# Performance work log

Measured on AMD Instinct MI355X. Metric: run time of the kernel, lower is better.

## Reference

```python
import jax, jax.numpy as jnp
import numpy as np

D_MODEL = 1024
N_HEADS = 16
HEAD_DIM = D_MODEL // N_HEADS
WINDOW = 256


def setup_inputs() -> dict:
    key = jax.random.key(0)
    k1, k2, k3 = jax.random.split(key, 3)
    B, T = 4, 2048
    x = jax.random.normal(k1, (B, T, D_MODEL), dtype=jnp.float32)
    # weights stored as [in, out] (torch Linear does x @ W.T with W [out,in])
    scale_qkv = 1.0 / np.sqrt(D_MODEL)
    w_qkv = jax.random.normal(k2, (D_MODEL, 3 * D_MODEL), dtype=jnp.float32) * scale_qkv
    w_out = jax.random.normal(k3, (D_MODEL, D_MODEL), dtype=jnp.float32) * scale_qkv
    return {"x": x, "w_qkv": w_qkv, "w_out": w_out}


def _sliding_window_attention(x, w_qkv, w_out):
    B, T, C = x.shape
    qkv = x @ w_qkv                              # [B,T,3C]
    q, k, v = jnp.split(qkv, 3, axis=-1)

    def reshape(t):
        return t.reshape(B, T, N_HEADS, HEAD_DIM).transpose(0, 2, 1, 3)  # [B,H,T,Dh]

    q, k, v = reshape(q), reshape(k), reshape(v)

    # banded causal mask: position i attends to j in [i-WINDOW, i]
    pos = jnp.arange(T)
    dist = pos[None, :] - pos[:, None]           # dist[i,j] = j - i
    blocked = (dist > 0) | (dist < -WINDOW)      # True = blocked

    scale = 1.0 / np.sqrt(HEAD_DIM)
    scores = jnp.einsum('bhqd,bhkd->bhqk', q, k) * scale
    scores = jnp.where(blocked[None, None], -jnp.inf, scores)
    attn = jax.nn.softmax(scores, axis=-1)
    out = jnp.einsum('bhqk,bhkd->bhqd', attn, v)
    out = out.transpose(0, 2, 1, 3).reshape(B, T, C)
    return out @ w_out


def reference(x, w_qkv, w_out):
    return _sliding_window_attention(x, w_qkv, w_out)
```

## Files before the change

### kernel.cpp

```cpp
#include <hip/hip_runtime.h>
#include <stdint.h>

#define D_MODEL 1024
#define NHEADS  16
#define WINDOW  256
#define BATCH   4
#define SEQ     2048
#define NROWS   (BATCH*SEQ)

using short8 = __attribute__((ext_vector_type(8))) short;
using f32x4  = __attribute__((ext_vector_type(4))) float;
using u32x4  = __attribute__((ext_vector_type(4))) uint32_t;
using u16x4  = __attribute__((ext_vector_type(4))) unsigned short;
typedef unsigned short u16;

__device__ __forceinline__ u16 f2b(float f) {
  union { float f; uint32_t u; } v; v.f = f;
  uint32_t r = v.u + 0x7fffu + ((v.u >> 16) & 1u);
  return (u16)(r >> 16);
}

__device__ __forceinline__ void gload_lds16(const void* g, void* l) {
  __builtin_amdgcn_global_load_lds(
      (const __attribute__((address_space(1))) uint32_t*)g,
      (__attribute__((address_space(3))) uint32_t*)l, 16, 0, 0);
}

__global__ void cvt_cast_kernel(const float* __restrict__ in, u16* __restrict__ out, int n4) {
  int i = blockIdx.x * blockDim.x + threadIdx.x;
  if (i < n4) {
    f32x4 v = *(const f32x4*)(in + 4 * (size_t)i);
    u16x4 o;
    o.x = f2b(v.x); o.y = f2b(v.y); o.z = f2b(v.z); o.w = f2b(v.w);
    *(u16x4*)(out + 4 * (size_t)i) = o;
  }
}

__global__ __launch_bounds__(256) void cvtT_kernel(const float* __restrict__ in, u16* __restrict__ out,
                                                   int K, int C) {
  __shared__ float T[64 * 65];
  const int nbn = C >> 6;
  const int bn = blockIdx.x % nbn, bk = blockIdx.x / nbn;
  const int tid = threadIdx.x;
#pragma unroll
  for (int it = 0; it < 4; ++it) {
    int c = it * 256 + tid;
    int k = c >> 4, g = c & 15;
    f32x4 v = *(const f32x4*)&in[(size_t)(bk * 64 + k) * C + bn * 64 + g * 4];
#pragma unroll
    for (int j = 0; j < 4; ++j) T[k * 65 + g * 4 + j] = v[j];
  }
  __syncthreads();
#pragma unroll
  for (int it = 0; it < 4; ++it) {
    int c = it * 256 + tid;
    int n = c >> 4, kg = c & 15;
    u16x4 o;
#pragma unroll
    for (int j = 0; j < 4; ++j) o[j] = f2b(T[(kg * 4 + j) * 65 + n]);
    *(u16x4*)&out[(size_t)(bn * 64 + n) * K + bk * 64 + kg * 4] = o;
  }
}

template <int MODE>
__global__ __launch_bounds__(256) void gemm97_kernel(
    const u16* __restrict__ A, const u16* __restrict__ BT,
    u16* __restrict__ qk, u16* __restrict__ vT, float* __restrict__ outf,
    int M, int N, int K, int nbx) {
  __shared__ short SM[3 * 8192];

  const int tid = threadIdx.x;
  const int l = tid & 63;
  const int w = tid >> 6;
  const int lr = l & 15, g = l >> 4;
  const int wr = w >> 1, wc = w & 1;

  const int nwg = gridDim.x;
  const int lid = blockIdx.x;
  const int wg = (lid & 7) * (nwg >> 3) + (lid >> 3);
  const int bx = wg % nbx, by = wg / nbx;
  const int m0 = by * 128, n0 = bx * 128;

  const int ko = (g ^ (lr & 3)) * 8;
  const int NKT = K >> 5;

  const int c0 = tid, c1 = 256 + tid;
  const int r0 = c0 >> 2, g0 = (c0 & 3) ^ (r0 & 3);
  const int r1 = c1 >> 2, g1 = (c1 & 3) ^ (r1 & 3);

  f32x4 acc[4][4] = {};

  auto stage = [&](int slot, int kt) {
    const int kk = kt << 5;
    short* As = SM + slot * 8192;
    short* Bs = As + 4096;
    gload_lds16(A  + (size_t)(m0 + r0) * K + kk + g0 * 8, &As[(w * 64) * 8]);
    gload_lds16(A  + (size_t)(m0 + r1) * K + kk + g1 * 8, &As[(256 + w * 64) * 8]);
    gload_lds16(BT + (size_t)(n0 + r0) * K + kk + g0 * 8, &Bs[(w * 64) * 8]);
    gload_lds16(BT + (size_t)(n0 + r1) * K + kk + g1 * 8, &Bs[(256 + w * 64) * 8]);
  };

  stage(0, 0);
  stage(1, 1);

  int slot = 0;
  for (int t = 0; t < NKT; ++t) {
    if (t == NKT - 1) { asm volatile("s_waitcnt vmcnt(0)" ::: "memory"); }
    else              { asm volatile("s_waitcnt vmcnt(4)" ::: "memory"); }
    __builtin_amdgcn_s_barrier();
    if (t + 2 < NKT) {
      int s2 = slot + 2; if (s2 >= 3) s2 -= 3;
      stage(s2, t + 2);
    }
    const short* As = SM + slot * 8192;
    const short* Bs = As + 4096;
    short8 af[4], bf[4];
#pragma unroll
    for (int fm = 0; fm < 4; ++fm)
      af[fm] = *(const short8*)&As[(wr * 64 + fm * 16 + lr) * 32 + ko];
#pragma unroll
    for (int fn = 0; fn < 4; ++fn)
      bf[fn] = *(const short8*)&Bs[(wc * 64 + fn * 16 + lr) * 32 + ko];
#pragma unroll
    for (int fm = 0; fm < 4; ++fm)
#pragma unroll
      for (int fn = 0; fn < 4; ++fn)
        acc[fm][fn] = __builtin_amdgcn_mfma_f32_16x16x32_bf16(af[fm], bf[fn], acc[fm][fn], 0, 0, 0);
    slot = (slot + 1 == 3) ? 0 : slot + 1;
  }

  if (MODE == 1) {
#pragma unroll
    for (int fm = 0; fm < 4; ++fm) {
      const int m = m0 + wr * 64 + fm * 16 + (l >> 4) * 4;
#pragma unroll
      for (int fn = 0; fn < 4; ++fn) {
        const int n = n0 + wc * 64 + fn * 16 + lr;
#pragma unroll
        for (int r = 0; r < 4; ++r)
          outf[(size_t)(m + r) * N + n] = acc[fm][fn][r];
      }
    }
    return;
  }

  if (n0 < 2048) {
#pragma unroll
    for (int fm = 0; fm < 4; ++fm) {
      const int m = m0 + wr * 64 + fm * 16 + (l >> 4) * 4;
#pragma unroll
      for (int fn = 0; fn < 4; ++fn) {
        const int n = n0 + wc * 64 + fn * 16 + lr;
#pragma unroll
        for (int r = 0; r < 4; ++r)
          qk[(size_t)(m + r) * 2048 + n] = f2b(acc[fm][fn][r]);
      }
    }
  } else {
    __syncthreads();
    short* Tw = SM + w * 1152;
    const int b = by >> 4;
    const int h = (n0 - 2048 + wc * 64) >> 6;
    const int t0 = (by & 15) * 128 + wr * 64;
    const size_t dbase = ((size_t)(b * NHEADS + h)) * 64;
#pragma unroll
    for (int fn = 0; fn < 4; ++fn) {
#pragma unroll
      for (int fm = 0; fm < 4; ++fm)
#pragma unroll
        for (int r = 0; r < 4; ++r)
          Tw[lr * 72 + fm * 16 + (l >> 4) * 4 + r] = (short)f2b(acc[fm][fn][r]);
      asm volatile("s_waitcnt lgkmcnt(0)" ::: "memory");
#pragma unroll
      for (int it = 0; it < 2; ++it) {
        int c = it * 64 + l;
        int row = c >> 3, off = (c & 7) * 8;
        short8 v = *(const short8*)&Tw[row * 72 + off];
        *(short8*)&vT[(dbase + fn * 16 + row) * 2048 + t0 + off] = v;
      }
      asm volatile("s_waitcnt lgkmcnt(0)" ::: "memory");
    }
  }
}

__global__ __launch_bounds__(256) void attn_kernel(
    const u16* __restrict__ qk, const u16* __restrict__ vT, u16* __restrict__ attn) {
  __shared__ short Ks[2][64 * 72];
  __shared__ short Vs[2][64 * 72];
  __shared__ short Ps[4 * 16 * 72];

  const int tid = threadIdx.x;
  const int l = tid & 63;
  const int w = tid >> 6;

  const int lid = blockIdx.x;
  const int xcd = lid & 7, slot = lid >> 3;
  const int bh = (slot >> 5) * 8 + xcd;
  const int qt = slot & 31;
  const int b = bh >> 4, h = bh & 15;
  const int qbase = qt * 64;
  const size_t rowbase = (size_t)b * 2048;
  const int lr = l & 15, lk = (l >> 4) * 8;

  const int row0 = tid >> 3,          off0 = (tid & 7) * 8;
  const int row1 = (256 + tid) >> 3,  off1 = ((256 + tid) & 7) * 8;

  u32x4 kreg0, kreg1, vreg0, vreg1;
  auto load_regs = [&](int kt) {
    const int kbase = kt * 64;
    kreg0 = *(const u32x4*)&qk[(rowbase + kbase + row0) * 2048 + 1024 + h * 64 + off0];
    kreg1 = *(const u32x4*)&qk[(rowbase + kbase + row1) * 2048 + 1024 + h * 64 + off1];
    vreg0 = *(const u32x4*)&vT[((size_t)bh * 64 + row0) * 2048 + kbase + off0];
    vreg1 = *(const u32x4*)&vT[((size_t)bh * 64 + row1) * 2048 + kbase + off1];
  };
  auto write_lds = [&](int buf) {
    *(u32x4*)&Ks[buf][row0 * 72 + off0] = kreg0;
    *(u32x4*)&Ks[buf][row1 * 72 + off1] = kreg1;
    *(u32x4*)&Vs[buf][row0 * 72 + off0] = vreg0;
    *(u32x4*)&Vs[buf][row1 * 72 + off1] = vreg1;
  };

  const size_t qrowg = (rowbase + qbase + w * 16 + lr) * 2048 + h * 64;
  short8 aq0 = *(const short8*)&qk[qrowg + lk];
  short8 aq1 = *(const short8*)&qk[qrowg + 32 + lk];

  float lsum[4] = {0.f, 0.f, 0.f, 0.f};
  f32x4 o[4] = {};

  int kt0 = qt - 4; if (kt0 < 0) kt0 = 0;

  load_regs(kt0);
  write_lds(0);
  if (kt0 + 1 <= qt) load_regs(kt0 + 1);
  asm volatile("s_waitcnt lgkmcnt(0)" ::: "memory");
  __builtin_amdgcn_s_barrier();

  int cur = 0;
  for (int kt = kt0; kt <= qt; ++kt) {
    const int kbase = kt * 64;

    f32x4 s[4] = {};
    __builtin_amdgcn_s_setprio(1);
#pragma unroll
    for (int fn = 0; fn < 4; ++fn) {
      short8 bk0 = *(const short8*)&Ks[cur][(fn * 16 + lr) * 72 + lk];
      short8 bk1 = *(const short8*)&Ks[cur][(fn * 16 + lr) * 72 + 32 + lk];
      s[fn] = __builtin_amdgcn_mfma_f32_16x16x32_bf16(aq0, bk0, s[fn], 0, 0, 0);
      s[fn] = __builtin_amdgcn_mfma_f32_16x16x32_bf16(aq1, bk1, s[fn], 0, 0, 0);
    }
    __builtin_amdgcn_s_setprio(0);

    f32x4 p[4];
    if (kt == qt || kt == qt - 4) {
      const int qrow0 = qbase + w * 16 + (l >> 4) * 4;
#pragma unroll
      for (int fn = 0; fn < 4; ++fn) {
        int kj = kbase + fn * 16 + lr;
#pragma unroll
        for (int r = 0; r < 4; ++r) {
          int qi = qrow0 + r;
          bool ok = (kj <= qi) && (kj >= qi - WINDOW);
          p[fn][r] = ok ? __expf(s[fn][r] * 0.125f) : 0.f;
        }
      }
    } else {
#pragma unroll
      for (int fn = 0; fn < 4; ++fn)
#pragma unroll
        for (int r = 0; r < 4; ++r)
          p[fn][r] = __expf(s[fn][r] * 0.125f);
    }
#pragma unroll
    for (int r = 0; r < 4; ++r)
      lsum[r] += (p[0][r] + p[1][r]) + (p[2][r] + p[3][r]);

    short* Pw = &Ps[w * 16 * 72];
#pragma unroll
    for (int fn = 0; fn < 4; ++fn)
#pragma unroll
      for (int r = 0; r < 4; ++r)
        Pw[((l >> 4) * 4 + r) * 72 + fn * 16 + lr] = (short)f2b(p[fn][r]);
    asm volatile("s_waitcnt lgkmcnt(0)" ::: "memory");

    __builtin_amdgcn_s_setprio(1);
#pragma unroll
    for (int ks = 0; ks < 2; ++ks) {
      short8 pa = *(const short8*)&Pw[lr * 72 + ks * 32 + lk];
#pragma unroll
      for (int fd = 0; fd < 4; ++fd) {
        short8 vb = *(const short8*)&Vs[cur][(fd * 16 + lr) * 72 + ks * 32 + lk];
        o[fd] = __builtin_amdgcn_mfma_f32_16x16x32_bf16(pa, vb, o[fd], 0, 0, 0);
      }
    }
    __builtin_amdgcn_s_setprio(0);
    asm volatile("s_waitcnt lgkmcnt(0)" ::: "memory");

    if (kt + 1 <= qt) {
      write_lds(cur ^ 1);
      if (kt + 2 <= qt) load_regs(kt + 2);
      asm volatile("s_waitcnt lgkmcnt(0)" ::: "memory");
      __builtin_amdgcn_s_barrier();
      cur ^= 1;
    }
  }

#pragma unroll
  for (int off = 1; off < 16; off <<= 1)
#pragma unroll
    for (int r = 0; r < 4; ++r) lsum[r] += __shfl_xor(lsum[r], off);

#pragma unroll
  for (int fd = 0; fd < 4; ++fd) {
#pragma unroll
    for (int r = 0; r < 4; ++r) {
      int m = qbase + w * 16 + (l >> 4) * 4 + r;
      float val = o[fd][r] / lsum[r];
      attn[(rowbase + m) * 1024 + h * 64 + fd * 16 + lr] = f2b(val);
    }
  }
}

extern "C" void kernel_launch(void* const* d_in, const int* in_sizes, int n_in,
                              void* d_out, int out_size, void* d_ws, size_t ws_size,
                              hipStream_t stream) {
  const float* x     = (const float*)d_in[0];
  const float* w_qkv = (const float*)d_in[1];
  const float* w_out = (const float*)d_in[2];
  float* out = (float*)d_out;
  uint8_t* ws = (uint8_t*)d_ws;

  u16* xb    = (u16*)(ws + 0);
  u16* wqkvT = (u16*)(ws + 16777216);
  u16* woutT = (u16*)(ws + 23068672);
  u16* qk    = (u16*)(ws + 25165824);
  u16* vT    = (u16*)(ws + 58720256);

  cvt_cast_kernel<<<(NROWS * D_MODEL / 4 + 255) / 256, 256, 0, stream>>>(x, xb, NROWS * D_MODEL / 4);
  cvtT_kernel<<<(3 * D_MODEL / 64) * (D_MODEL / 64), 256, 0, stream>>>(w_qkv, wqkvT, D_MODEL, 3 * D_MODEL);
  cvtT_kernel<<<(D_MODEL / 64) * (D_MODEL / 64), 256, 0, stream>>>(w_out, woutT, D_MODEL, D_MODEL);

  gemm97_kernel<0><<<(3 * D_MODEL / 128) * (NROWS / 128), 256, 0, stream>>>(
      xb, wqkvT, qk, vT, nullptr, NROWS, 3 * D_MODEL, D_MODEL, 3 * D_MODEL / 128);

  attn_kernel<<<BATCH * NHEADS * (SEQ / 64), 256, 0, stream>>>(qk, vT, xb);

  gemm97_kernel<1><<<(D_MODEL / 128) * (NROWS / 128), 256, 0, stream>>>(
      xb, woutT, nullptr, nullptr, out, NROWS, D_MODEL, D_MODEL, D_MODEL / 128);
}
```

Baseline: 136.4 us.

## Process two query tiles per attention block to share K/V tile loads

Each attention workgroup now computes two adjacent 64-row query tiles, iterating over the union of their key windows and reusing each staged K/V tile for both. This reduces global K/V traffic and LDS staging per query row and halves the grid size. It costs extra registers for the second set of accumulators and query fragments, and fewer workgroups to spread across CUs.

```diff
diff --git a/kernel.cpp b/kernel.cpp
--- a/kernel.cpp
+++ b/kernel.cpp
@@ -195,10 +195,10 @@
 
   const int lid = blockIdx.x;
   const int xcd = lid & 7, slot = lid >> 3;
-  const int bh = (slot >> 5) * 8 + xcd;
-  const int qt = slot & 31;
+  const int bh = (slot >> 4) * 8 + xcd;
+  const int qt2 = slot & 15;
+  const int qtA = qt2 * 2, qtB = qtA + 1;
   const int b = bh >> 4, h = bh & 15;
-  const int qbase = qt * 64;
   const size_t rowbase = (size_t)b * 2048;
   const int lr = l & 15, lk = (l >> 4) * 8;
 
@@ -220,84 +220,94 @@
     *(u32x4*)&Vs[buf][row1 * 72 + off1] = vreg1;
   };
 
-  const size_t qrowg = (rowbase + qbase + w * 16 + lr) * 2048 + h * 64;
-  short8 aq0 = *(const short8*)&qk[qrowg + lk];
-  short8 aq1 = *(const short8*)&qk[qrowg + 32 + lk];
-
-  float lsum[4] = {0.f, 0.f, 0.f, 0.f};
-  f32x4 o[4] = {};
-
-  int kt0 = qt - 4; if (kt0 < 0) kt0 = 0;
-
-  load_regs(kt0);
+  const size_t qrgA = (rowbase + qtA * 64 + w * 16 + lr) * 2048 + h * 64;
+  const size_t qrgB = (rowbase + qtB * 64 + w * 16 + lr) * 2048 + h * 64;
+  short8 aqA0 = *(const short8*)&qk[qrgA + lk];
+  short8 aqA1 = *(const short8*)&qk[qrgA + 32 + lk];
+  short8 aqB0 = *(const short8*)&qk[qrgB + lk];
+  short8 aqB1 = *(const short8*)&qk[qrgB + 32 + lk];
+
+  float lsumA[4] = {0.f, 0.f, 0.f, 0.f};
+  float lsumB[4] = {0.f, 0.f, 0.f, 0.f};
+  f32x4 oA[4] = {};
+  f32x4 oB[4] = {};
+
+  int ktlo = qtA - 4; if (ktlo < 0) ktlo = 0;
+  const int kthi = qtB;
+
+  load_regs(ktlo);
   write_lds(0);
-  if (kt0 + 1 <= qt) load_regs(kt0 + 1);
+  load_regs(ktlo + 1);
   asm volatile("s_waitcnt lgkmcnt(0)" ::: "memory");
   __builtin_amdgcn_s_barrier();
 
+  short* Pw = &Ps[w * 16 * 72];
   int cur = 0;
-  for (int kt = kt0; kt <= qt; ++kt) {
+  for (int kt = ktlo; kt <= kthi; ++kt) {
     const int kbase = kt * 64;
 
-    f32x4 s[4] = {};
-    __builtin_amdgcn_s_setprio(1);
-#pragma unroll
-    for (int fn = 0; fn < 4; ++fn) {
-      short8 bk0 = *(const short8*)&Ks[cur][(fn * 16 + lr) * 72 + lk];
-      short8 bk1 = *(const short8*)&Ks[cur][(fn * 16 + lr) * 72 + 32 + lk];
-      s[fn] = __builtin_amdgcn_mfma_f32_16x16x32_bf16(aq0, bk0, s[fn], 0, 0, 0);
-      s[fn] = __builtin_amdgcn_mfma_f32_16x16x32_bf16(aq1, bk1, s[fn], 0, 0, 0);
-    }
-    __builtin_amdgcn_s_setprio(0);
-
-    f32x4 p[4];
-    if (kt == qt || kt == qt - 4) {
-      const int qrow0 = qbase + w * 16 + (l >> 4) * 4;
-#pragma unroll
-      for (int fn = 0; fn < 4; ++fn) {
-        int kj = kbase + fn * 16 + lr;
-#pragma unroll
-        for (int r = 0; r < 4; ++r) {
-          int qi = qrow0 + r;
-          bool ok = (kj <= qi) && (kj >= qi - WINDOW);
-          p[fn][r] = ok ? __expf(s[fn][r] * 0.125f) : 0.f;
-        }
-      }
-    } else {
-#pragma unroll
-      for (int fn = 0; fn < 4; ++fn)
-#pragma unroll
-        for (int r = 0; r < 4; ++r)
-          p[fn][r] = __expf(s[fn][r] * 0.125f);
-    }
-#pragma unroll
-    for (int r = 0; r < 4; ++r)
-      lsum[r] += (p[0][r] + p[1][r]) + (p[2][r] + p[3][r]);
-
-    short* Pw = &Ps[w * 16 * 72];
-#pragma unroll
-    for (int fn = 0; fn < 4; ++fn)
-#pragma unroll
-      for (int r = 0; r < 4; ++r)
-        Pw[((l >> 4) * 4 + r) * 72 + fn * 16 + lr] = (short)f2b(p[fn][r]);
-    asm volatile("s_waitcnt lgkmcnt(0)" ::: "memory");
-
-    __builtin_amdgcn_s_setprio(1);
-#pragma unroll
-    for (int ks = 0; ks < 2; ++ks) {
-      short8 pa = *(const short8*)&Pw[lr * 72 + ks * 32 + lk];
-#pragma unroll
-      for (int fd = 0; fd < 4; ++fd) {
-        short8 vb = *(const short8*)&Vs[cur][(fd * 16 + lr) * 72 + ks * 32 + lk];
-        o[fd] = __builtin_amdgcn_mfma_f32_16x16x32_bf16(pa, vb, o[fd], 0, 0, 0);
-      }
-    }
-    __builtin_amdgcn_s_setprio(0);
-    asm volatile("s_waitcnt lgkmcnt(0)" ::: "memory");
-
-    if (kt + 1 <= qt) {
+#define DO_SUB(AQ0, AQ1, OARR, LSUM, QTX)                                                   \
+    {                                                                                       \
+      f32x4 s[4] = {};                                                                      \
+      __builtin_amdgcn_s_setprio(1);                                                        \
+      _Pragma("unroll")                                                                     \
+      for (int fn = 0; fn < 4; ++fn) {                                                      \
+        short8 bk0 = *(const short8*)&Ks[cur][(fn * 16 + lr) * 72 + lk];                    \
+        short8 bk1 = *(const short8*)&Ks[cur][(fn * 16 + lr) * 72 + 32 + lk];               \
+        s[fn] = __builtin_amdgcn_mfma_f32_16x16x32_bf16(AQ0, bk0, s[fn], 0, 0, 0);          \
+        s[fn] = __builtin_amdgcn_mfma_f32_16x16x32_bf16(AQ1, bk1, s[fn], 0, 0, 0);          \
+      }                                                                                     \
+      __builtin_amdgcn_s_setprio(0);                                                        \
+      f32x4 p[4];                                                                           \
+      if (kt == (QTX) || kt == (QTX) - 4) {                                                 \
+        const int qrow0 = (QTX) * 64 + w * 16 + (l >> 4) * 4;                               \
+        _Pragma("unroll")                                                                   \
+        for (int fn = 0; fn < 4; ++fn) {                                                    \
+          int kj = kbase + fn * 16 + lr;                                                    \
+          _Pragma("unroll")                                                                 \
+          for (int r = 0; r < 4; ++r) {                                                     \
+            int qi = qrow0 + r;                                                             \
+            bool ok = (kj <= qi) && (kj >= qi - WINDOW);                                    \
+            p[fn][r] = ok ? __expf(s[fn][r] * 0.125f) : 0.f;                                \
+          }                                                                                 \
+        }                                                                                   \
+      } else {                                                                              \
+        _Pragma("unroll")                                                                   \
+        for (int fn = 0; fn < 4; ++fn)                                                      \
+          _Pragma("unroll")                                                                 \
+          for (int r = 0; r < 4; ++r)                                                       \
+            p[fn][r] = __expf(s[fn][r] * 0.125f);                                           \
+      }                                                                                     \
+      _Pragma("unroll")                                                                     \
+      for (int r = 0; r < 4; ++r)                                                           \
+        (LSUM)[r] += (p[0][r] + p[1][r]) + (p[2][r] + p[3][r]);                             \
+      _Pragma("unroll")                                                                     \
+      for (int fn = 0; fn < 4; ++fn)                                                        \
+        _Pragma("unroll")                                                                   \
+        for (int r = 0; r < 4; ++r)                                                         \
+          Pw[((l >> 4) * 4 + r) * 72 + fn * 16 + lr] = (short)f2b(p[fn][r]);                \
+      asm volatile("s_waitcnt lgkmcnt(0)" ::: "memory");                                    \
+      __builtin_amdgcn_s_setprio(1);                                                        \
+      _Pragma("unroll")                                                                     \
+      for (int ks = 0; ks < 2; ++ks) {                                                      \
+        short8 pa = *(const short8*)&Pw[lr * 72 + ks * 32 + lk];                            \
+        _Pragma("unroll")                                                                   \
+        for (int fd = 0; fd < 4; ++fd) {                                                    \
+          short8 vb = *(const short8*)&Vs[cur][(fd * 16 + lr) * 72 + ks * 32 + lk];         \
+          (OARR)[fd] = __builtin_amdgcn_mfma_f32_16x16x32_bf16(pa, vb, (OARR)[fd], 0, 0, 0);\
+        }                                                                                   \
+      }                                                                                     \
+      __builtin_amdgcn_s_setprio(0);                                                        \
+      asm volatile("s_waitcnt lgkmcnt(0)" ::: "memory");                                    \
+    }
+
+    if (kt <= qtA)      DO_SUB(aqA0, aqA1, oA, lsumA, qtA)
+    if (kt >= qtA - 3)  DO_SUB(aqB0, aqB1, oB, lsumB, qtB)
+#undef DO_SUB
+
+    if (kt + 1 <= kthi) {
       write_lds(cur ^ 1);
-      if (kt + 2 <= qt) load_regs(kt + 2);
+      if (kt + 2 <= kthi) load_regs(kt + 2);
       asm volatile("s_waitcnt lgkmcnt(0)" ::: "memory");
       __builtin_amdgcn_s_barrier();
       cur ^= 1;
@@ -307,15 +317,19 @@
 #pragma unroll
   for (int off = 1; off < 16; off <<= 1)
 #pragma unroll
-    for (int r = 0; r < 4; ++r) lsum[r] += __shfl_xor(lsum[r], off);
+    for (int r = 0; r < 4; ++r) {
+      lsumA[r] += __shfl_xor(lsumA[r], off);
+      lsumB[r] += __shfl_xor(lsumB[r], off);
+    }
 
 #pragma unroll
   for (int fd = 0; fd < 4; ++fd) {
 #pragma unroll
     for (int r = 0; r < 4; ++r) {
-      int m = qbase + w * 16 + (l >> 4) * 4 + r;
-      float val = o[fd][r] / lsum[r];
-      attn[(rowbase + m) * 1024 + h * 64 + fd * 16 + lr] = f2b(val);
+      int mA = qtA * 64 + w * 16 + (l >> 4) * 4 + r;
+      int mB = qtB * 64 + w * 16 + (l >> 4) * 4 + r;
+      attn[(rowbase + mA) * 1024 + h * 64 + fd * 16 + lr] = f2b(oA[fd][r] / lsumA[r]);
+      attn[(rowbase + mB) * 1024 + h * 64 + fd * 16 + lr] = f2b(oB[fd][r] / lsumB[r]);
     }
   }
 }
@@ -342,7 +356,7 @@
   gemm97_kernel<0><<<(3 * D_MODEL / 128) * (NROWS / 128), 256, 0, stream>>>(
       xb, wqkvT, qk, vT, nullptr, NROWS, 3 * D_MODEL, D_MODEL, 3 * D_MODEL / 128);
 
-  attn_kernel<<<BATCH * NHEADS * (SEQ / 64), 256, 0, stream>>>(qk, vT, xb);
+  attn_kernel<<<BATCH * NHEADS * (SEQ / 128), 256, 0, stream>>>(qk, vT, xb);
 
   gemm97_kernel<1><<<(D_MODEL / 128) * (NROWS / 128), 256, 0, stream>>>(
       xb, woutT, nullptr, nullptr, out, NROWS, D_MODEL, D_MODEL, D_MODEL / 128);
```

After: 139.1 us. About the same (+2.0%).

## Enlarge GEMM tile to 256x128 with 8 waves and BK=64 split-stage pipeline

Applied to the files above, without the earlier changes.

Replaces the 128x128, 4-wave GEMM with a 256x128 tile run by 512 threads (8 waves), a K-step of 64 and an XOR swizzle over 8 groups. Loads for the next stage are split into A and B halves and interleaved with the two k-halves of MFMA work, with extra barriers and s_setprio raised around the MFMA blocks. The aim is more data reuse per global load and better overlap of loads with compute. In exchange it uses more LDS (144KB), adds a barrier per k-half, and launches half as many workgroups.

```diff
diff --git a/kernel.cpp b/kernel.cpp
--- a/kernel.cpp
+++ b/kernel.cpp
@@ -63,82 +63,100 @@
 }
 
 template <int MODE>
-__global__ __launch_bounds__(256) void gemm97_kernel(
+__global__ __launch_bounds__(512, 2) void gemm256_kernel(
     const u16* __restrict__ A, const u16* __restrict__ BT,
     u16* __restrict__ qk, u16* __restrict__ vT, float* __restrict__ outf,
     int M, int N, int K, int nbx) {
-  __shared__ short SM[3 * 8192];
+  __shared__ short SM[3 * 24576];
 
   const int tid = threadIdx.x;
   const int l = tid & 63;
   const int w = tid >> 6;
-  const int lr = l & 15, g = l >> 4;
-  const int wr = w >> 1, wc = w & 1;
+  const int wm = w >> 1, wn = w & 1;
+  const int lr = l & 15, q = l >> 4;
+  const int gsw = lr & 7;
 
   const int nwg = gridDim.x;
   const int lid = blockIdx.x;
   const int wg = (lid & 7) * (nwg >> 3) + (lid >> 3);
   const int bx = wg % nbx, by = wg / nbx;
-  const int m0 = by * 128, n0 = bx * 128;
-
-  const int ko = (g ^ (lr & 3)) * 8;
-  const int NKT = K >> 5;
-
-  const int c0 = tid, c1 = 256 + tid;
-  const int r0 = c0 >> 2, g0 = (c0 & 3) ^ (r0 & 3);
-  const int r1 = c1 >> 2, g1 = (c1 & 3) ^ (r1 & 3);
+  const int m0 = by * 256, n0 = bx * 128;
+
+  const int NT = K >> 6;
 
   f32x4 acc[4][4] = {};
 
-  auto stage = [&](int slot, int kt) {
-    const int kk = kt << 5;
-    short* As = SM + slot * 8192;
-    short* Bs = As + 4096;
-    gload_lds16(A  + (size_t)(m0 + r0) * K + kk + g0 * 8, &As[(w * 64) * 8]);
-    gload_lds16(A  + (size_t)(m0 + r1) * K + kk + g1 * 8, &As[(256 + w * 64) * 8]);
-    gload_lds16(BT + (size_t)(n0 + r0) * K + kk + g0 * 8, &Bs[(w * 64) * 8]);
-    gload_lds16(BT + (size_t)(n0 + r1) * K + kk + g1 * 8, &Bs[(256 + w * 64) * 8]);
+  auto stageA = [&](int slot, int kt) {
+    short* As = SM + slot * 24576;
+#pragma unroll
+    for (int i = 0; i < 4; ++i) {
+      int c = i * 512 + tid;
+      int row = c >> 3;
+      int gs = (c & 7) ^ (row & 7);
+      gload_lds16(A + (size_t)(m0 + row) * K + (kt << 6) + gs * 8,
+                  &As[(i * 512 + w * 64) * 8]);
+    }
   };
-
-  stage(0, 0);
-  stage(1, 1);
+  auto stageB = [&](int slot, int kt) {
+    short* Bs = SM + slot * 24576 + 16384;
+#pragma unroll
+    for (int i = 0; i < 2; ++i) {
+      int c = i * 512 + tid;
+      int row = c >> 3;
+      int gs = (c & 7) ^ (row & 7);
+      gload_lds16(BT + (size_t)(n0 + row) * K + (kt << 6) + gs * 8,
+                  &Bs[(i * 512 + w * 64) * 8]);
+    }
+  };
+
+  stageA(0, 0); stageB(0, 0);
+  stageA(1, 1); stageB(1, 1);
 
   int slot = 0;
-  for (int t = 0; t < NKT; ++t) {
-    if (t == NKT - 1) { asm volatile("s_waitcnt vmcnt(0)" ::: "memory"); }
-    else              { asm volatile("s_waitcnt vmcnt(4)" ::: "memory"); }
+  for (int t = 0; t < NT; ++t) {
+    if (t + 1 < NT) { asm volatile("s_waitcnt vmcnt(6)" ::: "memory"); }
+    else            { asm volatile("s_waitcnt vmcnt(0)" ::: "memory"); }
     __builtin_amdgcn_s_barrier();
-    if (t + 2 < NKT) {
-      int s2 = slot + 2; if (s2 >= 3) s2 -= 3;
-      stage(s2, t + 2);
-    }
-    const short* As = SM + slot * 8192;
-    const short* Bs = As + 4096;
-    short8 af[4], bf[4];
-#pragma unroll
-    for (int fm = 0; fm < 4; ++fm)
-      af[fm] = *(const short8*)&As[(wr * 64 + fm * 16 + lr) * 32 + ko];
-#pragma unroll
-    for (int fn = 0; fn < 4; ++fn)
-      bf[fn] = *(const short8*)&Bs[(wc * 64 + fn * 16 + lr) * 32 + ko];
-#pragma unroll
-    for (int fm = 0; fm < 4; ++fm)
-#pragma unroll
-      for (int fn = 0; fn < 4; ++fn)
-        acc[fm][fn] = __builtin_amdgcn_mfma_f32_16x16x32_bf16(af[fm], bf[fn], acc[fm][fn], 0, 0, 0);
+
+    const short* As = SM + slot * 24576;
+    const short* Bs = As + 16384;
+    int s2 = slot + 2; if (s2 >= 3) s2 -= 3;
+    const bool st = (t + 2 < NT);
+
+#pragma unroll
+    for (int kh = 0; kh < 2; ++kh) {
+      short8 af[4], bfr[4];
+      const int ko = (((kh << 2) | q) ^ gsw) * 8;
+#pragma unroll
+      for (int mf = 0; mf < 4; ++mf)
+        af[mf] = *(const short8*)&As[(wm * 64 + mf * 16 + lr) * 64 + ko];
+#pragma unroll
+      for (int nf = 0; nf < 4; ++nf)
+        bfr[nf] = *(const short8*)&Bs[(wn * 64 + nf * 16 + lr) * 64 + ko];
+      if (st) { if (kh == 0) stageA(s2, t + 2); else stageB(s2, t + 2); }
+      __builtin_amdgcn_s_barrier();
+      asm volatile("s_waitcnt lgkmcnt(0)" ::: "memory");
+      __builtin_amdgcn_s_setprio(1);
+#pragma unroll
+      for (int mf = 0; mf < 4; ++mf)
+#pragma unroll
+        for (int nf = 0; nf < 4; ++nf)
+          acc[mf][nf] = __builtin_amdgcn_mfma_f32_16x16x32_bf16(af[mf], bfr[nf], acc[mf][nf], 0, 0, 0);
+      __builtin_amdgcn_s_setprio(0);
+    }
     slot = (slot + 1 == 3) ? 0 : slot + 1;
   }
 
   if (MODE == 1) {
 #pragma unroll
-    for (int fm = 0; fm < 4; ++fm) {
-      const int m = m0 + wr * 64 + fm * 16 + (l >> 4) * 4;
-#pragma unroll
-      for (int fn = 0; fn < 4; ++fn) {
-        const int n = n0 + wc * 64 + fn * 16 + lr;
+    for (int mf = 0; mf < 4; ++mf) {
+      const int m = m0 + wm * 64 + mf * 16 + q * 4;
+#pragma unroll
+      for (int nf = 0; nf < 4; ++nf) {
+        const int n = n0 + wn * 64 + nf * 16 + lr;
 #pragma unroll
         for (int r = 0; r < 4; ++r)
-          outf[(size_t)(m + r) * N + n] = acc[fm][fn][r];
+          outf[(size_t)(m + r) * N + n] = acc[mf][nf][r];
       }
     }
     return;
@@ -146,37 +164,37 @@
 
   if (n0 < 2048) {
 #pragma unroll
-    for (int fm = 0; fm < 4; ++fm) {
-      const int m = m0 + wr * 64 + fm * 16 + (l >> 4) * 4;
-#pragma unroll
-      for (int fn = 0; fn < 4; ++fn) {
-        const int n = n0 + wc * 64 + fn * 16 + lr;
+    for (int mf = 0; mf < 4; ++mf) {
+      const int m = m0 + wm * 64 + mf * 16 + q * 4;
+#pragma unroll
+      for (int nf = 0; nf < 4; ++nf) {
+        const int n = n0 + wn * 64 + nf * 16 + lr;
 #pragma unroll
         for (int r = 0; r < 4; ++r)
-          qk[(size_t)(m + r) * 2048 + n] = f2b(acc[fm][fn][r]);
+          qk[(size_t)(m + r) * 2048 + n] = f2b(acc[mf][nf][r]);
       }
     }
   } else {
     __syncthreads();
     short* Tw = SM + w * 1152;
-    const int b = by >> 4;
-    const int h = (n0 - 2048 + wc * 64) >> 6;
-    const int t0 = (by & 15) * 128 + wr * 64;
-    const size_t dbase = ((size_t)(b * NHEADS + h)) * 64;
-#pragma unroll
-    for (int fn = 0; fn < 4; ++fn) {
-#pragma unroll
-      for (int fm = 0; fm < 4; ++fm)
+    const int b = by >> 3;
+    const int head = (n0 - 2048 + wn * 64) >> 6;
+    const int t0 = (by & 7) * 256 + wm * 64;
+    const size_t dbase = ((size_t)(b * NHEADS + head)) * 64;
+#pragma unroll
+    for (int nf = 0; nf < 4; ++nf) {
+#pragma unroll
+      for (int mf = 0; mf < 4; ++mf)
 #pragma unroll
         for (int r = 0; r < 4; ++r)
-          Tw[lr * 72 + fm * 16 + (l >> 4) * 4 + r] = (short)f2b(acc[fm][fn][r]);
+          Tw[lr * 72 + mf * 16 + q * 4 + r] = (short)f2b(acc[mf][nf][r]);
       asm volatile("s_waitcnt lgkmcnt(0)" ::: "memory");
 #pragma unroll
       for (int it = 0; it < 2; ++it) {
         int c = it * 64 + l;
         int row = c >> 3, off = (c & 7) * 8;
         short8 v = *(const short8*)&Tw[row * 72 + off];
-        *(short8*)&vT[(dbase + fn * 16 + row) * 2048 + t0 + off] = v;
+        *(short8*)&vT[(dbase + nf * 16 + row) * 2048 + t0 + off] = v;
       }
       asm volatile("s_waitcnt lgkmcnt(0)" ::: "memory");
     }
@@ -339,11 +357,11 @@
   cvtT_kernel<<<(3 * D_MODEL / 64) * (D_MODEL / 64), 256, 0, stream>>>(w_qkv, wqkvT, D_MODEL, 3 * D_MODEL);
   cvtT_kernel<<<(D_MODEL / 64) * (D_MODEL / 64), 256, 0, stream>>>(w_out, woutT, D_MODEL, D_MODEL);
 
-  gemm97_kernel<0><<<(3 * D_MODEL / 128) * (NROWS / 128), 256, 0, stream>>>(
+  gemm256_kernel<0><<<(3 * D_MODEL / 128) * (NROWS / 256), 512, 0, stream>>>(
       xb, wqkvT, qk, vT, nullptr, NROWS, 3 * D_MODEL, D_MODEL, 3 * D_MODEL / 128);
 
   attn_kernel<<<BATCH * NHEADS * (SEQ / 64), 256, 0, stream>>>(qk, vT, xb);
 
-  gemm97_kernel<1><<<(D_MODEL / 128) * (NROWS / 128), 256, 0, stream>>>(
+  gemm256_kernel<1><<<(D_MODEL / 128) * (NROWS / 256), 512, 0, stream>>>(
       xb, woutT, nullptr, nullptr, out, NROWS, D_MODEL, D_MODEL, D_MODEL / 128);
 }
```

New measurement: 128.2 us. 1.06x faster.
